# Performance work log

Measured on AMD Instinct MI355X. Metric: run time of the kernel, lower is better.

The kernel has to match this reference:

```python
import jax, jax.numpy as jnp
import numpy as np

# dims: batch N, queries Q, frames F, patches-per-frame L, heads H, head_dim D
N, Q, F, L, H, D = 32, 64, 16, 196, 12, 64
E = H * D          # embed_dim = 768
K = F * L          # kv length = 3136


def setup_inputs() -> dict:
    key = jax.random.key(0)
    kq, kk, kv, km, kw1, kw2 = jax.random.split(key, 6)
    q = jax.random.normal(kq, (N, Q, E), dtype=jnp.float32)
    k = jax.random.normal(kk, (N, K, H, D), dtype=jnp.float32)
    v = jax.random.normal(kv, (N, K, H, D), dtype=jnp.float32)
    # frame-padding mask; guarantee >=1 valid patch per frame so the
    # per-frame softmax never sees an all -inf group (NaN otherwise)
    m = jax.random.bernoulli(km, 0.9, (N, K))
    m = m.reshape(N, F, L).at[:, :, 0].set(True).reshape(N, K)
    W_in = jax.random.normal(kw1, (E, E), dtype=jnp.float32) * 0.02   # in_proj (n_act=1)
    W_out = jax.random.normal(kw2, (E, E), dtype=jnp.float32) * 0.02  # out_proj
    return {"q": q, "k": k, "v": v, "m": m, "W_in": W_in, "W_out": W_out}


def reference(q, k, v, m, W_in, W_out):
    n, nq, e = q.shape
    h, d = H, e // H
    # in_proj (no bias) then split into heads; n_act == 1 so qs has one element
    qs = (q @ W_in.T).reshape(n, nq, h, d)
    # scaled QK affinity: [n, Q, K, h]
    aff = jnp.einsum('nqhc,nkhc->nqkh', qs * (d ** -0.5), k)
    # frame mask broadcast over queries and heads
    aff = jnp.where(m[:, None, :, None], aff, -jnp.inf)
    kn = aff.shape[2]
    # grouped softmax over patches within each frame (dim=-2 of the view)
    aff = jax.nn.softmax(aff.reshape(n, nq, F, kn // F, h), axis=-2)
    aff = aff.reshape(n, nq, kn, h)
    # mix with v and output projection
    mix = jnp.einsum('nqlh,nlhc->nqhc', aff, v)
    out = mix.reshape(n, nq, e) @ W_out.T
    # second return: stacked flattened qs, shape [n, n_act=1, Q, E]
    qs_out = qs.reshape(n, nq, e)[:, None]
    return out, qs_out
```

## Files before the change

kernel.cpp:

```cpp
#include <hip/hip_runtime.h>
#include <hip/hip_bf16.h>
#include <cfloat>

#define N_B 32
#define QN 64
#define FN 16
#define LP 196
#define HN 12
#define DH 64
#define EE 768
#define KLEN 3136
#define FPB 2
#define KROWS 208
#define VST 256

typedef short s16x4 __attribute__((ext_vector_type(4)));
typedef __bf16 bf16x4 __attribute__((ext_vector_type(4)));
typedef __bf16 bf16x8 __attribute__((ext_vector_type(8)));
typedef float f32x4 __attribute__((ext_vector_type(4)));
typedef unsigned u32x2 __attribute__((ext_vector_type(2)));

__device__ __forceinline__ bf16x8 cvt8(f32x4 a, f32x4 b) {
    bf16x8 r;
    r[0] = (__bf16)a[0]; r[1] = (__bf16)a[1]; r[2] = (__bf16)a[2]; r[3] = (__bf16)a[3];
    r[4] = (__bf16)b[0]; r[5] = (__bf16)b[1]; r[6] = (__bf16)b[2]; r[7] = (__bf16)b[3];
    return r;
}
__device__ __forceinline__ unsigned short bfb(float x) {
    return __builtin_bit_cast(unsigned short, (__bf16)x);
}
__device__ __forceinline__ unsigned pkbf(float lo, float hi) {
    return (unsigned)bfb(lo) | ((unsigned)bfb(hi) << 16);
}

__device__ __forceinline__ f32x4 mfma16(s16x4 a, s16x4 b, f32x4 c) {
#if __has_builtin(__builtin_amdgcn_mfma_f32_16x16x16_bf16)
    return __builtin_amdgcn_mfma_f32_16x16x16_bf16(__builtin_bit_cast(bf16x4, a),
                                                   __builtin_bit_cast(bf16x4, b), c, 0, 0, 0);
#elif __has_builtin(__builtin_amdgcn_mfma_f32_16x16x16bf16_1k)
    return __builtin_amdgcn_mfma_f32_16x16x16bf16_1k(a, b, c, 0, 0, 0);
#else
    f32x4 d;
    asm volatile("v_mfma_f32_16x16x16_bf16 %0, %1, %2, %3"
                 : "=v"(d) : "v"(a), "v"(b), "v"(c));
    return d;
#endif
}

__global__ __launch_bounds__(256) void gemm_mfma(const float* __restrict__ A,
                                                 const float* __restrict__ W,
                                                 float* __restrict__ C) {
    __shared__ unsigned short As[64 * 72];
    __shared__ unsigned short Ws[48 * 72];
    const int t = threadIdx.x;
    const int w = t >> 6, lane = t & 63, lr = lane & 15, lg = lane >> 4;
    const int m0 = blockIdx.x * 64;
    const int n0 = blockIdx.y * 48;

    f32x4 acc[3];
#pragma unroll
    for (int ct = 0; ct < 3; ++ct) acc[ct] = (f32x4){0.f, 0.f, 0.f, 0.f};

    for (int k0 = 0; k0 < EE; k0 += 32) {
        {
            int row = t >> 2, cb = t & 3;
            const float* src = A + (size_t)(m0 + row) * EE + k0 + cb * 8;
            f32x4 a = *(const f32x4*)src, b = *(const f32x4*)(src + 4);
            *(bf16x8*)&As[row * 72 + cb * 8] = cvt8(a, b);
        }
        if (t < 192) {
            int row = t >> 2, cb = t & 3;
            const float* src = W + (size_t)(n0 + row) * EE + k0 + cb * 8;
            f32x4 a = *(const f32x4*)src, b = *(const f32x4*)(src + 4);
            *(bf16x8*)&Ws[row * 72 + cb * 8] = cvt8(a, b);
        }
        __syncthreads();
        bf16x8 a = *(const bf16x8*)&As[(w * 16 + lr) * 72 + lg * 8];
#pragma unroll
        for (int ct = 0; ct < 3; ++ct) {
            bf16x8 b = *(const bf16x8*)&Ws[(ct * 16 + lr) * 72 + lg * 8];
            acc[ct] = __builtin_amdgcn_mfma_f32_16x16x32_bf16(a, b, acc[ct], 0, 0, 0);
        }
        __syncthreads();
    }
#pragma unroll
    for (int ct = 0; ct < 3; ++ct)
#pragma unroll
        for (int r = 0; r < 4; ++r)
            C[(size_t)(m0 + w * 16 + lg * 4 + r) * EE + n0 + ct * 16 + lr] = acc[ct][r];
}

__global__ __launch_bounds__(256) void zero_f32(float* __restrict__ p, int n4) {
    int i = blockIdx.x * 256 + threadIdx.x;
    if (i < n4) ((float4*)p)[i] = make_float4(0.f, 0.f, 0.f, 0.f);
}

__global__ __launch_bounds__(256, 2) void attn_mfma(const float* __restrict__ qs_g,
                                                    const float* __restrict__ k_g,
                                                    const float* __restrict__ v_g,
                                                    const int* __restrict__ m_g,
                                                    float* __restrict__ mix_g) {
    const int h = blockIdx.x, fg = blockIdx.y, n = blockIdx.z;

    __shared__ __attribute__((aligned(16))) unsigned short KV_s[64 * VST];
    __shared__ __attribute__((aligned(16))) float bias_s[224];

    const int t = threadIdx.x;
    const int w = t >> 6, lane = t & 63, lr = lane & 15, lg = lane >> 4;

    bf16x8 qb0, qb1;
    {
        const float* qp = qs_g + ((size_t)n * QN + w * 16 + lr) * EE + h * DH + lg * 8;
        f32x4 a = *(const f32x4*)qp, b = *(const f32x4*)(qp + 4);
        f32x4 c = *(const f32x4*)(qp + 32), d = *(const f32x4*)(qp + 36);
#pragma unroll
        for (int i = 0; i < 4; ++i) { a[i] *= 0.125f; b[i] *= 0.125f; c[i] *= 0.125f; d[i] *= 0.125f; }
        qb0 = cvt8(a, b);
        qb1 = cvt8(c, d);
    }

    float mix[4][4];
#pragma unroll
    for (int dt = 0; dt < 4; ++dt)
#pragma unroll
        for (int r = 0; r < 4; ++r) mix[dt][r] = 0.f;

    for (int ff = 0; ff < FPB; ++ff) {
        const size_t kbase = (size_t)n * KLEN + (size_t)(fg * FPB + ff) * LP;

        __syncthreads();

#pragma unroll
        for (int u = 0; u < 7; ++u) {
            int unit = t + 256 * u;
            if (unit < KROWS * 8) {
                int p = unit >> 3, blk = unit & 7;
                f32x4 a = {0.f, 0.f, 0.f, 0.f}, b = {0.f, 0.f, 0.f, 0.f};
                if (p < LP) {
                    const float* src = k_g + ((kbase + p) * HN + h) * DH + blk * 8;
                    a = *(const f32x4*)src;
                    b = *(const f32x4*)(src + 4);
                }
                *(bf16x8*)&KV_s[p * 64 + ((blk ^ (p & 7)) << 3)] = cvt8(a, b);
            }
        }
        if (t < 224) {
            float bv = -1e30f;
            if (t < LP && m_g[kbase + t] != 0) bv = 0.f;
            bias_s[t] = bv;
        }
        __syncthreads();

        f32x4 sc[13];
        __builtin_amdgcn_s_setprio(1);
#pragma unroll
        for (int tl = 0; tl < 13; ++tl) {
            int row = tl * 16 + lr;
            bf16x8 a0 = *(const bf16x8*)&KV_s[row * 64 + ((lg ^ (lr & 7)) << 3)];
            bf16x8 a1 = *(const bf16x8*)&KV_s[row * 64 + (((4 + lg) ^ (lr & 7)) << 3)];
            f32x4 z = {0.f, 0.f, 0.f, 0.f};
            z = __builtin_amdgcn_mfma_f32_16x16x32_bf16(a0, qb0, z, 0, 0, 0);
            sc[tl] = __builtin_amdgcn_mfma_f32_16x16x32_bf16(a1, qb1, z, 0, 0, 0);
        }
        __builtin_amdgcn_s_setprio(0);

        f32x4 va[4], vb[4];
#pragma unroll
        for (int u = 0; u < 4; ++u) {
            int unit = t + 256 * u;
            int pp = unit >> 3, d4 = unit & 7;
            int p0 = pp * 2;
            va[u] = (f32x4){0.f, 0.f, 0.f, 0.f};
            vb[u] = (f32x4){0.f, 0.f, 0.f, 0.f};
            if (p0 < LP) {
                const float* vg = v_g + ((kbase + p0) * HN + h) * DH + d4 * 4;
                va[u] = *(const f32x4*)vg;
                if (p0 + 1 < LP) vb[u] = *(const f32x4*)(vg + (size_t)HN * DH);
            }
        }

        float mx = -FLT_MAX;
#pragma unroll
        for (int tl = 0; tl < 13; ++tl) {
            f32x4 bv = *(const f32x4*)&bias_s[tl * 16 + lg * 4];
#pragma unroll
            for (int r = 0; r < 4; ++r) {
                float sv = sc[tl][r] + bv[r];
                sc[tl][r] = sv;
                mx = fmaxf(mx, sv);
            }
        }
        mx = fmaxf(mx, __shfl_xor(mx, 16));
        mx = fmaxf(mx, __shfl_xor(mx, 32));
        float sum = 0.f;
        unsigned pk[13][2];
#pragma unroll
        for (int tl = 0; tl < 13; ++tl) {
            float e0 = __expf(sc[tl][0] - mx);
            float e1 = __expf(sc[tl][1] - mx);
            float e2 = __expf(sc[tl][2] - mx);
            float e3 = __expf(sc[tl][3] - mx);
            sum += (e0 + e1) + (e2 + e3);
            pk[tl][0] = pkbf(e0, e1);
            pk[tl][1] = pkbf(e2, e3);
        }
        sum += __shfl_xor(sum, 16);
        sum += __shfl_xor(sum, 32);
        float inv = 1.0f / sum;
        float li[4];
#pragma unroll
        for (int r = 0; r < 4; ++r) li[r] = __shfl(inv, lg * 4 + r);

        __syncthreads();

#pragma unroll
        for (int u = 0; u < 4; ++u) {
            int unit = t + 256 * u;
            int pp = unit >> 3, d4 = unit & 7;
            int p0 = pp * 2;
            if (p0 < KROWS) {
                int blk = p0 >> 3, sub = p0 & 7;
#pragma unroll
                for (int i = 0; i < 4; ++i) {
                    int row = d4 * 4 + i;
                    int g = (row + 2 * (row >> 2)) & 7;
                    *(unsigned*)&KV_s[row * VST + (((blk ^ g) << 3) | sub)] = pkbf(va[u][i], vb[u][i]);
                }
            }
        }
#pragma unroll
        for (int u = 0; u < 4; ++u) {
            int unit = t + 256 * u;
            int pp = unit >> 3, d4 = unit & 7;
            int p0 = pp * 2;
            va[u] = (f32x4){0.f, 0.f, 0.f, 0.f};
            vb[u] = (f32x4){0.f, 0.f, 0.f, 0.f};
            if (p0 < LP) {
                const float* vg = v_g + ((kbase + p0) * HN + h) * DH + (8 + d4) * 4;
                va[u] = *(const f32x4*)vg;
                if (p0 + 1 < LP) vb[u] = *(const f32x4*)(vg + (size_t)HN * DH);
            }
        }
        __syncthreads();

        f32x4 pv[4];
#pragma unroll
        for (int dt = 0; dt < 4; ++dt) pv[dt] = (f32x4){0.f, 0.f, 0.f, 0.f};
        __builtin_amdgcn_s_setprio(1);
#pragma unroll
        for (int dt = 0; dt < 2; ++dt) {
            int row = dt * 16 + lr;
            int g = (row + 2 * (row >> 2)) & 7;
#pragma unroll
            for (int kt = 0; kt < 13; ++kt) {
                int c0 = kt * 16 + lg * 4;
                s16x4 b = *(const s16x4*)&KV_s[row * VST + ((((c0 >> 3) ^ g) << 3) | (c0 & 7))];
                s16x4 a = __builtin_bit_cast(s16x4, (u32x2){pk[kt][0], pk[kt][1]});
                pv[dt] = mfma16(a, b, pv[dt]);
            }
        }
        __builtin_amdgcn_s_setprio(0);

#pragma unroll
        for (int u = 0; u < 4; ++u) {
            int unit = t + 256 * u;
            int pp = unit >> 3, d4 = unit & 7;
            int p0 = pp * 2;
            if (p0 < KROWS) {
                int blk = p0 >> 3, sub = p0 & 7;
#pragma unroll
                for (int i = 0; i < 4; ++i) {
                    int row = 32 + d4 * 4 + i;
                    int g = (row + 2 * (row >> 2)) & 7;
                    *(unsigned*)&KV_s[row * VST + (((blk ^ g) << 3) | sub)] = pkbf(va[u][i], vb[u][i]);
                }
            }
        }
        __syncthreads();

        __builtin_amdgcn_s_setprio(1);
#pragma unroll
        for (int dt = 2; dt < 4; ++dt) {
            int row = dt * 16 + lr;
            int g = (row + 2 * (row >> 2)) & 7;
#pragma unroll
            for (int kt = 0; kt < 13; ++kt) {
                int c0 = kt * 16 + lg * 4;
                s16x4 b = *(const s16x4*)&KV_s[row * VST + ((((c0 >> 3) ^ g) << 3) | (c0 & 7))];
                s16x4 a = __builtin_bit_cast(s16x4, (u32x2){pk[kt][0], pk[kt][1]});
                pv[dt] = mfma16(a, b, pv[dt]);
            }
        }
        __builtin_amdgcn_s_setprio(0);

#pragma unroll
        for (int dt = 0; dt < 4; ++dt)
#pragma unroll
            for (int r = 0; r < 4; ++r) mix[dt][r] += pv[dt][r] * li[r];
    }

#pragma unroll
    for (int dt = 0; dt < 4; ++dt)
#pragma unroll
        for (int r = 0; r < 4; ++r)
            atomicAdd(mix_g + ((size_t)n * QN + w * 16 + lg * 4 + r) * EE + h * DH + dt * 16 + lr,
                      mix[dt][r]);
}

extern "C" void kernel_launch(void* const* d_in, const int* in_sizes, int n_in,
                              void* d_out, int out_size, void* d_ws, size_t ws_size,
                              hipStream_t stream) {
    const float* q  = (const float*)d_in[0];
    const float* k  = (const float*)d_in[1];
    const float* v  = (const float*)d_in[2];
    const int*   m  = (const int*)d_in[3];
    const float* Wi = (const float*)d_in[4];
    const float* Wo = (const float*)d_in[5];

    float* out = (float*)d_out;
    float* qs  = out + (size_t)N_B * QN * EE;
    float* mix = (float*)d_ws;

    const int mix_n4 = (N_B * QN * EE) / 4;
    dim3 ggrid((N_B * QN) / 64, EE / 48);
    gemm_mfma<<<ggrid, 256, 0, stream>>>(q, Wi, qs);
    zero_f32<<<(mix_n4 + 255) / 256, 256, 0, stream>>>(mix, mix_n4);
    attn_mfma<<<dim3(HN, FN / FPB, N_B), 256, 0, stream>>>(qs, k, v, m, mix);
    gemm_mfma<<<ggrid, 256, 0, stream>>>(mix, Wo, out);
}
```

Baseline: 218.0 us.

## Split K and V shared buffers, hoist all loads, cut per-frame barriers

Gives K and transposed V their own shared-memory buffers instead of reusing one. All K, V and mask global loads for a frame are now issued together up front, so there are two barriers per frame instead of four. The softmax probabilities are normalized in fp32 before packing to bf16, and the PV MFMAs accumulate straight into the running mix, which removes the cross-lane shuffle of inverse sums. In exchange, more registers are held live (about 28 float4 loads at once) and LDS use per block is larger, which could limit occupancy or cause spills.

```diff
diff --git a/kernel.cpp b/kernel.cpp
--- a/kernel.cpp
+++ b/kernel.cpp
@@ -102,7 +102,8 @@
                                                     float* __restrict__ mix_g) {
     const int h = blockIdx.x, fg = blockIdx.y, n = blockIdx.z;
 
-    __shared__ __attribute__((aligned(16))) unsigned short KV_s[64 * VST];
+    __shared__ __attribute__((aligned(16))) unsigned short K_s[KROWS * 64];
+    __shared__ __attribute__((aligned(16))) unsigned short Vt_s[64 * VST];
     __shared__ __attribute__((aligned(16))) float bias_s[224];
 
     const int t = threadIdx.x;
@@ -130,45 +131,24 @@
 
         __syncthreads();
 
-#pragma unroll
-        for (int u = 0; u < 7; ++u) {
-            int unit = t + 256 * u;
-            if (unit < KROWS * 8) {
-                int p = unit >> 3, blk = unit & 7;
-                f32x4 a = {0.f, 0.f, 0.f, 0.f}, b = {0.f, 0.f, 0.f, 0.f};
-                if (p < LP) {
-                    const float* src = k_g + ((kbase + p) * HN + h) * DH + blk * 8;
-                    a = *(const f32x4*)src;
-                    b = *(const f32x4*)(src + 4);
-                }
-                *(bf16x8*)&KV_s[p * 64 + ((blk ^ (p & 7)) << 3)] = cvt8(a, b);
-            }
-        }
-        if (t < 224) {
-            float bv = -1e30f;
-            if (t < LP && m_g[kbase + t] != 0) bv = 0.f;
-            bias_s[t] = bv;
-        }
-        __syncthreads();
-
-        f32x4 sc[13];
-        __builtin_amdgcn_s_setprio(1);
-#pragma unroll
-        for (int tl = 0; tl < 13; ++tl) {
-            int row = tl * 16 + lr;
-            bf16x8 a0 = *(const bf16x8*)&KV_s[row * 64 + ((lg ^ (lr & 7)) << 3)];
-            bf16x8 a1 = *(const bf16x8*)&KV_s[row * 64 + (((4 + lg) ^ (lr & 7)) << 3)];
-            f32x4 z = {0.f, 0.f, 0.f, 0.f};
-            z = __builtin_amdgcn_mfma_f32_16x16x32_bf16(a0, qb0, z, 0, 0, 0);
-            sc[tl] = __builtin_amdgcn_mfma_f32_16x16x32_bf16(a1, qb1, z, 0, 0, 0);
-        }
-        __builtin_amdgcn_s_setprio(0);
-
-        f32x4 va[4], vb[4];
-#pragma unroll
-        for (int u = 0; u < 4; ++u) {
-            int unit = t + 256 * u;
-            int pp = unit >> 3, d4 = unit & 7;
+        f32x4 ka[7], kb[7];
+#pragma unroll
+        for (int u = 0; u < 7; ++u) {
+            int unit = t + 256 * u;
+            int p = unit >> 3, blk = unit & 7;
+            ka[u] = (f32x4){0.f, 0.f, 0.f, 0.f};
+            kb[u] = (f32x4){0.f, 0.f, 0.f, 0.f};
+            if (unit < KROWS * 8 && p < LP) {
+                const float* src = k_g + ((kbase + p) * HN + h) * DH + blk * 8;
+                ka[u] = *(const f32x4*)src;
+                kb[u] = *(const f32x4*)(src + 4);
+            }
+        }
+        f32x4 va[7], vb[7];
+#pragma unroll
+        for (int u = 0; u < 7; ++u) {
+            int unit = t + 256 * u;
+            int pp = unit >> 4, d4 = unit & 15;
             int p0 = pp * 2;
             va[u] = (f32x4){0.f, 0.f, 0.f, 0.f};
             vb[u] = (f32x4){0.f, 0.f, 0.f, 0.f};
@@ -178,6 +158,46 @@
                 if (p0 + 1 < LP) vb[u] = *(const f32x4*)(vg + (size_t)HN * DH);
             }
         }
+        int mr = (t < LP) ? m_g[kbase + t] : 0;
+
+#pragma unroll
+        for (int u = 0; u < 7; ++u) {
+            int unit = t + 256 * u;
+            if (unit < KROWS * 8) {
+                int p = unit >> 3, blk = unit & 7;
+                *(bf16x8*)&K_s[p * 64 + ((blk ^ (p & 7)) << 3)] = cvt8(ka[u], kb[u]);
+            }
+        }
+#pragma unroll
+        for (int u = 0; u < 7; ++u) {
+            int unit = t + 256 * u;
+            int pp = unit >> 4, d4 = unit & 15;
+            int p0 = pp * 2;
+            if (p0 < KROWS) {
+                int blk = p0 >> 3, sub = p0 & 7;
+#pragma unroll
+                for (int i = 0; i < 4; ++i) {
+                    int row = d4 * 4 + i;
+                    int g = (row + 2 * (row >> 2)) & 7;
+                    *(unsigned*)&Vt_s[row * VST + (((blk ^ g) << 3) | sub)] = pkbf(va[u][i], vb[u][i]);
+                }
+            }
+        }
+        if (t < 224) bias_s[t] = (t < LP && mr != 0) ? 0.f : -1e30f;
+        __syncthreads();
+
+        f32x4 sc[13];
+        __builtin_amdgcn_s_setprio(1);
+#pragma unroll
+        for (int tl = 0; tl < 13; ++tl) {
+            int row = tl * 16 + lr;
+            bf16x8 a0 = *(const bf16x8*)&K_s[row * 64 + ((lg ^ (lr & 7)) << 3)];
+            bf16x8 a1 = *(const bf16x8*)&K_s[row * 64 + (((4 + lg) ^ (lr & 7)) << 3)];
+            f32x4 z = {0.f, 0.f, 0.f, 0.f};
+            z = __builtin_amdgcn_mfma_f32_16x16x32_bf16(a0, qb0, z, 0, 0, 0);
+            sc[tl] = __builtin_amdgcn_mfma_f32_16x16x32_bf16(a1, qb1, z, 0, 0, 0);
+        }
+        __builtin_amdgcn_s_setprio(0);
 
         float mx = -FLT_MAX;
 #pragma unroll
@@ -193,7 +213,6 @@
         mx = fmaxf(mx, __shfl_xor(mx, 16));
         mx = fmaxf(mx, __shfl_xor(mx, 32));
         float sum = 0.f;
-        unsigned pk[13][2];
 #pragma unroll
         for (int tl = 0; tl < 13; ++tl) {
             float e0 = __expf(sc[tl][0] - mx);
@@ -201,102 +220,35 @@
             float e2 = __expf(sc[tl][2] - mx);
             float e3 = __expf(sc[tl][3] - mx);
             sum += (e0 + e1) + (e2 + e3);
-            pk[tl][0] = pkbf(e0, e1);
-            pk[tl][1] = pkbf(e2, e3);
+            sc[tl][0] = e0; sc[tl][1] = e1; sc[tl][2] = e2; sc[tl][3] = e3;
         }
         sum += __shfl_xor(sum, 16);
         sum += __shfl_xor(sum, 32);
         float inv = 1.0f / sum;
-        float li[4];
-#pragma unroll
-        for (int r = 0; r < 4; ++r) li[r] = __shfl(inv, lg * 4 + r);
-
-        __syncthreads();
-
-#pragma unroll
-        for (int u = 0; u < 4; ++u) {
-            int unit = t + 256 * u;
-            int pp = unit >> 3, d4 = unit & 7;
-            int p0 = pp * 2;
-            if (p0 < KROWS) {
-                int blk = p0 >> 3, sub = p0 & 7;
-#pragma unroll
-                for (int i = 0; i < 4; ++i) {
-                    int row = d4 * 4 + i;
-                    int g = (row + 2 * (row >> 2)) & 7;
-                    *(unsigned*)&KV_s[row * VST + (((blk ^ g) << 3) | sub)] = pkbf(va[u][i], vb[u][i]);
-                }
-            }
-        }
-#pragma unroll
-        for (int u = 0; u < 4; ++u) {
-            int unit = t + 256 * u;
-            int pp = unit >> 3, d4 = unit & 7;
-            int p0 = pp * 2;
-            va[u] = (f32x4){0.f, 0.f, 0.f, 0.f};
-            vb[u] = (f32x4){0.f, 0.f, 0.f, 0.f};
-            if (p0 < LP) {
-                const float* vg = v_g + ((kbase + p0) * HN + h) * DH + (8 + d4) * 4;
-                va[u] = *(const f32x4*)vg;
-                if (p0 + 1 < LP) vb[u] = *(const f32x4*)(vg + (size_t)HN * DH);
-            }
-        }
-        __syncthreads();
-
-        f32x4 pv[4];
-#pragma unroll
-        for (int dt = 0; dt < 4; ++dt) pv[dt] = (f32x4){0.f, 0.f, 0.f, 0.f};
+        unsigned pk[13][2];
+#pragma unroll
+        for (int tl = 0; tl < 13; ++tl) {
+            pk[tl][0] = pkbf(sc[tl][0] * inv, sc[tl][1] * inv);
+            pk[tl][1] = pkbf(sc[tl][2] * inv, sc[tl][3] * inv);
+        }
+
         __builtin_amdgcn_s_setprio(1);
 #pragma unroll
-        for (int dt = 0; dt < 2; ++dt) {
+        for (int dt = 0; dt < 4; ++dt) {
             int row = dt * 16 + lr;
             int g = (row + 2 * (row >> 2)) & 7;
+            f32x4 acc = {mix[dt][0], mix[dt][1], mix[dt][2], mix[dt][3]};
 #pragma unroll
             for (int kt = 0; kt < 13; ++kt) {
                 int c0 = kt * 16 + lg * 4;
-                s16x4 b = *(const s16x4*)&KV_s[row * VST + ((((c0 >> 3) ^ g) << 3) | (c0 & 7))];
+                s16x4 b = *(const s16x4*)&Vt_s[row * VST + ((((c0 >> 3) ^ g) << 3) | (c0 & 7))];
                 s16x4 a = __builtin_bit_cast(s16x4, (u32x2){pk[kt][0], pk[kt][1]});
-                pv[dt] = mfma16(a, b, pv[dt]);
-            }
+                acc = mfma16(a, b, acc);
+            }
+#pragma unroll
+            for (int r = 0; r < 4; ++r) mix[dt][r] = acc[r];
         }
         __builtin_amdgcn_s_setprio(0);
-
-#pragma unroll
-        for (int u = 0; u < 4; ++u) {
-            int unit = t + 256 * u;
-            int pp = unit >> 3, d4 = unit & 7;
-            int p0 = pp * 2;
-            if (p0 < KROWS) {
-                int blk = p0 >> 3, sub = p0 & 7;
-#pragma unroll
-                for (int i = 0; i < 4; ++i) {
-                    int row = 32 + d4 * 4 + i;
-                    int g = (row + 2 * (row >> 2)) & 7;
-                    *(unsigned*)&KV_s[row * VST + (((blk ^ g) << 3) | sub)] = pkbf(va[u][i], vb[u][i]);
-                }
-            }
-        }
-        __syncthreads();
-
-        __builtin_amdgcn_s_setprio(1);
-#pragma unroll
-        for (int dt = 2; dt < 4; ++dt) {
-            int row = dt * 16 + lr;
-            int g = (row + 2 * (row >> 2)) & 7;
-#pragma unroll
-            for (int kt = 0; kt < 13; ++kt) {
-                int c0 = kt * 16 + lg * 4;
-                s16x4 b = *(const s16x4*)&KV_s[row * VST + ((((c0 >> 3) ^ g) << 3) | (c0 & 7))];
-                s16x4 a = __builtin_bit_cast(s16x4, (u32x2){pk[kt][0], pk[kt][1]});
-                pv[dt] = mfma16(a, b, pv[dt]);
-            }
-        }
-        __builtin_amdgcn_s_setprio(0);
-
-#pragma unroll
-        for (int dt = 0; dt < 4; ++dt)
-#pragma unroll
-            for (int r = 0; r < 4; ++r) mix[dt][r] += pv[dt][r] * li[r];
     }
 
 #pragma unroll
```

New measurement: 207.0 us. 5.0% less time.
